# Performance work log

Measured on AMD Instinct MI355X. Metric: run time of the kernel, lower is better.

Reference implementation:

```python
import jax, jax.numpy as jnp
import numpy as np

VOCAB = 50257
K = 10  # accuracy_slack_size


def setup_inputs() -> dict:
    key = jax.random.key(0)
    k1, k2, k3, k4 = jax.random.split(key, 4)
    logits = jax.random.normal(k1, (4, 2048, 512), dtype=jnp.float32)
    target = jax.random.randint(k2, (4, 2048), 0, VOCAB, dtype=jnp.int64 if jax.config.jax_enable_x64 else jnp.int32)
    mask = jax.random.randint(k3, (4, 2048), 0, 2, dtype=jnp.int32)
    W = jax.random.normal(k4, (512, VOCAB), dtype=jnp.float32) * 0.02
    b = jnp.zeros((VOCAB,), dtype=jnp.float32)
    return {"logits": logits, "target": target, "mask": mask, "W": W, "b": b}


def reference(logits, target, mask, W, b):
    N = logits.shape[0] * logits.shape[1]
    x = logits.reshape(N, logits.shape[-1])            # [N, d]
    # sampled_softmax.log_prob: full log-softmax over vocab
    logp = jax.nn.log_softmax(x @ W + b, axis=-1)      # [N, V]
    _, words = jax.lax.top_k(logp, K)                  # [N, K] indices
    tgt = target.reshape(-1)                           # [N]
    msk = mask.reshape(-1).astype(jnp.float32)         # [N]
    # vectorized membership: is target among top-K predictions?
    hit = jnp.any(words == tgt[:, None], axis=1).astype(jnp.float32)
    counter = jnp.sum(hit * msk)
    all_counter = jnp.sum(msk)
    return jnp.array([counter / all_counter])
```

## Files before the change

### kernel.cpp

```cpp
#include <hip/hip_runtime.h>
#include <stdint.h>

#define V_VOCAB 50257
#define V_PAD   51200
#define NROWS   8192
#define DIM     512
#define KTOP    10
#define ACH     16

typedef __attribute__((ext_vector_type(8))) short  short8;
typedef __attribute__((ext_vector_type(4))) float  f32x4;
typedef __attribute__((ext_vector_type(4))) int    i32x4;
typedef __attribute__((ext_vector_type(2))) unsigned int u32x2;

struct Ctrl { int mc; int namb; int hits; int pad_; };

#define OFF_WT8    0ULL
#define SZ_WT8     26214400ULL
#define OFF_XQ8    (OFF_WT8 + SZ_WT8)
#define SZ_XQ8     4194304ULL
#define OFF_BPAD   (OFF_XQ8 + SZ_XQ8)
#define SZ_COL     (51200ULL*4)
#define OFF_SW8    (OFF_BPAD + SZ_COL)
#define OFF_W1     (OFF_SW8 + SZ_COL)
#define OFF_IVW    (OFF_W1 + SZ_COL)
#define OFF_ROWIDX (OFF_IVW + SZ_COL)
#define OFF_SXR    (OFF_ROWIDX + 32768ULL)
#define OFF_X1     (OFF_SXR + 32768ULL)
#define OFF_RMETA  (OFF_X1 + 32768ULL)
#define OFF_COUNTS (OFF_RMETA + 131072ULL)
#define OFF_AMB    (OFF_COUNTS + 32768ULL)
#define OFF_CTRL   (OFF_AMB + 32768ULL)
#define OFF_RK     (OFF_CTRL + 16ULL)
#define OFF_SST    (OFF_RK + 32768ULL)

#define GLOAD16(gp, lp) __builtin_amdgcn_global_load_lds( \
    (const __attribute__((address_space(1))) unsigned int*)(gp), \
    (__attribute__((address_space(3))) unsigned int*)(lp), 16, 0, 0)

__global__ void k_prep(const int* __restrict__ mask, const float* __restrict__ b,
                       float* __restrict__ bpad, int* __restrict__ rowidx,
                       Ctrl* __restrict__ ctrl) {
  int i = blockIdx.x * 256 + threadIdx.x;
  if (i < V_PAD) bpad[i] = (i < V_VOCAB) ? b[i] : -1e30f;
  if (i < NROWS && mask[i] != 0) {
    int p = atomicAdd(&ctrl->mc, 1);
    rowidx[p] = i;
  }
}

__global__ void k_wstat(const float* __restrict__ W, float* __restrict__ sw8,
                        float* __restrict__ w1, float* __restrict__ invw) {
  const int j = blockIdx.x * 256 + threadIdx.x;
  if (j >= V_PAD) return;
  if (j >= V_VOCAB) { sw8[j] = 1.f; w1[j] = 0.f; invw[j] = 0.f; return; }
  float am = 0.f, s1 = 0.f;
  for (int k = 0; k < DIM; ++k) {
    float v = fabsf(W[(size_t)k * V_VOCAB + j]);
    am = fmaxf(am, v);
    s1 += v;
  }
  sw8[j] = (am > 0.f) ? am / 126.f : 1.f;
  invw[j] = (am > 0.f) ? 126.f / am : 0.f;
  w1[j] = s1;
}

__global__ void k_twt8(const float* __restrict__ W, const float* __restrict__ invw,
                       signed char* __restrict__ Wt8) {
  __shared__ float lt[64][65];
  const int vbase = blockIdx.x * 64;
  const int kbase = blockIdx.y * 64;
  const int tid = threadIdx.x;
  const int krow = tid >> 6;
  const int col  = tid & 63;
  const int v    = vbase + col;
#pragma unroll
  for (int rr = 0; rr < 16; ++rr) {
    int kl = krow + rr * 4;
    float val = (v < V_VOCAB) ? W[(size_t)(kbase + kl) * V_VOCAB + v] : 0.0f;
    lt[kl][col] = val;
  }
  __syncthreads();
  const int vr = tid >> 3;
  const int kc = tid & 7;
#pragma unroll
  for (int p = 0; p < 2; ++p) {
    const int vl = p * 32 + vr;
    const float inv = invw[vbase + vl];
    unsigned int lo = 0, hi = 0;
#pragma unroll
    for (int j = 0; j < 4; ++j) {
      int q = (int)rintf(lt[kc * 8 + j][vl] * inv);
      lo |= ((unsigned int)(q & 255)) << (8 * j);
    }
#pragma unroll
    for (int j = 0; j < 4; ++j) {
      int q = (int)rintf(lt[kc * 8 + 4 + j][vl] * inv);
      hi |= ((unsigned int)(q & 255)) << (8 * j);
    }
    u32x2 t; t.x = lo; t.y = hi;
    *(u32x2*)(Wt8 + (size_t)(vbase + vl) * DIM + kbase + kc * 8) = t;
  }
}

__global__ void k_xq(const float* __restrict__ x, const int* __restrict__ rowidx,
                     const Ctrl* __restrict__ ctrl, signed char* __restrict__ Xq8,
                     float* __restrict__ sxr, float* __restrict__ x1) {
  const int wid = threadIdx.x >> 6, lane = threadIdx.x & 63;
  const int i = blockIdx.x * 4 + wid;
  const int mc = ctrl->mc;
  if (i >= mc) {
    u32x2 z; z.x = 0; z.y = 0;
    *(u32x2*)(Xq8 + (size_t)i * DIM + lane * 8) = z;
    if (lane == 0) { sxr[i] = 1.f; x1[i] = 0.f; }
    return;
  }
  const float* src = x + (size_t)rowidx[i] * DIM + lane * 8;
  float v[8];
  float am = 0.f, s1 = 0.f;
#pragma unroll
  for (int j = 0; j < 8; ++j) {
    v[j] = src[j];
    float a = fabsf(v[j]);
    am = fmaxf(am, a);
    s1 += a;
  }
#pragma unroll
  for (int d = 1; d < 64; d <<= 1) {
    am = fmaxf(am, __shfl_xor(am, d, 64));
    s1 += __shfl_xor(s1, d, 64);
  }
  const float sx  = (am > 0.f) ? am / 126.f : 1.f;
  const float inv = (am > 0.f) ? 126.f / am : 0.f;
  unsigned int lo = 0, hi = 0;
#pragma unroll
  for (int j = 0; j < 4; ++j) {
    int q = (int)rintf(v[j] * inv);
    lo |= ((unsigned int)(q & 255)) << (8 * j);
  }
#pragma unroll
  for (int j = 0; j < 4; ++j) {
    int q = (int)rintf(v[4 + j] * inv);
    hi |= ((unsigned int)(q & 255)) << (8 * j);
  }
  u32x2 t; t.x = lo; t.y = hi;
  *(u32x2*)(Xq8 + (size_t)i * DIM + lane * 8) = t;
  if (lane == 0) { sxr[i] = sx; x1[i] = s1; }
}

__global__ void k_that8(const signed char* __restrict__ Xq8,
                        const signed char* __restrict__ Wt8,
                        const float* __restrict__ bpad, const float* __restrict__ sw8,
                        const float* __restrict__ w1,
                        const float* __restrict__ sxr, const float* __restrict__ x1,
                        const int* __restrict__ rowidx, const int* __restrict__ target,
                        const Ctrl* __restrict__ ctrl, f32x4* __restrict__ rmeta) {
  const int wid = threadIdx.x >> 6, lane = threadIdx.x & 63;
  const int i = blockIdx.x * 4 + wid;
  const int mc = ctrl->mc;
  if (i >= mc) {
    if (lane == 0) { f32x4 rm; rm.x = 1.f; rm.y = 1e30f; rm.z = 0.f; rm.w = 0.f; rmeta[i] = rm; }
    return;
  }
  const int tg = target[rowidx[i]];
  u32x2 xq = *(const u32x2*)(Xq8 + (size_t)i * DIM + lane * 8);
  u32x2 wq = *(const u32x2*)(Wt8 + (size_t)tg * DIM + lane * 8);
  int d = 0;
#pragma unroll
  for (int j = 0; j < 4; ++j)
    d += (int)((signed char)(xq.x >> (8 * j))) * (int)((signed char)(wq.x >> (8 * j)));
#pragma unroll
  for (int j = 0; j < 4; ++j)
    d += (int)((signed char)(xq.y >> (8 * j))) * (int)((signed char)(wq.y >> (8 * j)));
#pragma unroll
  for (int dd = 1; dd < 64; dd <<= 1) d += __shfl_xor(d, dd, 64);
  if (lane == 0) {
    const float sx = sxr[i], sw = sw8[tg], xl1 = x1[i];
    f32x4 rm;
    rm.x = sx;
    rm.y = fmaf((float)d, sx * sw, bpad[tg]);
    rm.z = 0.5005f * (sx * w1[tg] + sw * xl1) + 128.5f * (sx * sw)
           + 1e-3f;
    rm.w = fmaf(128.5f, sx, 0.5005f * xl1);
    rmeta[i] = rm;
  }
}

__launch_bounds__(256, 4)
__global__ void k_count8(const signed char* __restrict__ Xq8,
                         const signed char* __restrict__ Wt8,
                         const float* __restrict__ bpad, const float* __restrict__ sw8,
                         const float* __restrict__ w1, const f32x4* __restrict__ rmeta,
                         const Ctrl* __restrict__ ctrl, unsigned int* __restrict__ counts) {
  const int mc = ctrl->mc;
  const int lin = blockIdx.x;
  const int xcd = lin & 7;
  const int idx = lin >> 3;
  const int mt  = xcd * 4 + (idx & 3);
  const int nt  = idx >> 2;
  const int nbase = nt * 64;

  __shared__ char lds[24576];

  const int tid  = threadIdx.x;
  const int lane = tid & 63;
  const int w    = tid >> 6;
  const int wr   = w >> 1;
  const int wc   = w & 1;

  const char* Bg = (const char*)Wt8 + (size_t)nbase * 512;
  const int r8   = tid >> 3;
  const int sws  = ((tid & 7) ^ (r8 & 7)) * 16;
  const int dst0 = tid * 16;

  const int fr = lane & 15;
  const int fq = lane >> 4;
  const int p0 = ((fq) ^ (fr & 7)) * 16;
  const int p1 = ((4 + fq) ^ (fr & 7)) * 16;

#define STAGE(Ag, kt) do {                                                     \
    const size_t _kb = (size_t)(kt) * 128;                                     \
    _Pragma("unroll") for (int _c = 0; _c < 4; ++_c)                           \
      GLOAD16((Ag) + (size_t)(_c * 32 + r8) * 512 + _kb + sws,                 \
              lds + _c * 4096 + dst0);                                         \
    _Pragma("unroll") for (int _c = 0; _c < 2; ++_c)                           \
      GLOAD16(Bg + (size_t)(_c * 32 + r8) * 512 + _kb + sws,                   \
              lds + 16384 + _c * 4096 + dst0);                                 \
  } while (0)

#define KTILE() do {                                                           \
    _Pragma("unroll") for (int _ks = 0; _ks < 2; ++_ks) {                      \
      const int _p = _ks ? p1 : p0;                                            \
      i32x4 a4[4], b2[2];                                                      \
      _Pragma("unroll") for (int _i = 0; _i < 4; ++_i)                         \
        a4[_i] = *(const i32x4*)(lds + (wr * 64 + _i * 16 + fr) * 128 + _p);   \
      _Pragma("unroll") for (int _i = 0; _i < 2; ++_i)                         \
        b2[_i] = *(const i32x4*)(lds + 16384 +                                 \
                                 (wc * 32 + _i * 16 + fr) * 128 + _p);         \
      __builtin_amdgcn_s_setprio(1);                                           \
      _Pragma("unroll") for (int _m = 0; _m < 4; ++_m)                         \
      _Pragma("unroll") for (int _n = 0; _n < 2; ++_n)                         \
        acc[_m][_n] = __builtin_amdgcn_mfma_i32_16x16x64_i8(                   \
            a4[_m], b2[_n], acc[_m][_n], 0, 0, 0);                             \
      __builtin_amdgcn_s_setprio(0);                                           \
    }                                                                          \
  } while (0)

  i32x4 acc[4][2];

  for (int mb = mt * 128; mb < mc; mb += 4096) {
    const char* Ag = (const char*)Xq8 + (size_t)mb * 512;
#pragma unroll
    for (int a = 0; a < 4; ++a)
#pragma unroll
      for (int c = 0; c < 2; ++c) acc[a][c] = (i32x4)0;

#pragma unroll
    for (int kt = 0; kt < 4; ++kt) {
      STAGE(Ag, kt);
      __syncthreads();
      KTILE();
      __syncthreads();
    }

    float bv[2], swc[2], w1c[2];
#pragma unroll
    for (int ni = 0; ni < 2; ++ni) {
      const int c = nbase + wc * 32 + ni * 16 + fr;
      bv[ni] = bpad[c]; swc[ni] = sw8[c]; w1c[ni] = w1[c];
    }

#pragma unroll
    for (int mi = 0; mi < 4; ++mi) {
#pragma unroll
      for (int r = 0; r < 4; ++r) {
        const int m = mb + wr * 64 + mi * 16 + fq * 4 + r;
        const f32x4 rm = rmeta[m];
        const float arr = 0.5005f * rm.x;
        unsigned int p = 0;
#pragma unroll
        for (int ni = 0; ni < 2; ++ni) {
          const float s  = fmaf((float)acc[mi][ni][r], rm.x * swc[ni], bv[ni]);
          const float mm = fmaf(arr, w1c[ni], fmaf(rm.w, swc[ni], rm.z));
          p += (s > rm.y - mm) ? 1u : 0u;
          p += (s > rm.y + mm) ? (1u << 16) : 0u;
        }
        int pi = (int)p;
#pragma unroll
        for (int d = 1; d < 16; d <<= 1) pi += __shfl_xor(pi, d, 64);
        if ((lane & 15) == 0) atomicAdd(&counts[m], (unsigned int)pi);
      }
    }
  }
#undef STAGE
#undef KTILE
}

__global__ void k_decide(const unsigned int* __restrict__ counts,
                         Ctrl* __restrict__ ctrl, int* __restrict__ amb) {
  const int i = blockIdx.x * 256 + threadIdx.x;
  if (i >= ctrl->mc) return;
  const unsigned int c = counts[i];
  const unsigned int lo = c & 0xFFFFu, hi = c >> 16;
  if (lo <= KTOP - 1) { atomicAdd(&ctrl->hits, 1); }
  else if (hi >= KTOP) {  }
  else { int p = atomicAdd(&ctrl->namb, 1); amb[p] = i; }
}

__global__ void k_fixt(const float* __restrict__ x, const float* __restrict__ W,
                       const float* __restrict__ b, const int* __restrict__ rowidx,
                       const int* __restrict__ target, const int* __restrict__ amb,
                       const Ctrl* __restrict__ ctrl, float* __restrict__ sst) {
  const int a = blockIdx.x * 64 + threadIdx.x;
  if (a >= ctrl->namb) return;
  const int n = rowidx[amb[a]];
  const int tg = target[n];
  float st = 0.f;
  for (int k = 0; k < DIM; ++k)
    st = fmaf(x[(size_t)n * DIM + k], W[(size_t)k * V_VOCAB + tg], st);
  sst[a] = st + b[tg];
}

__global__ void k_fixscan(const float* __restrict__ x, const float* __restrict__ W,
                          const float* __restrict__ b, const int* __restrict__ rowidx,
                          const int* __restrict__ target, const int* __restrict__ amb,
                          const float* __restrict__ sst, const Ctrl* __restrict__ ctrl,
                          int* __restrict__ rk) {
  __shared__ float sx[ACH][DIM];
  const int j = blockIdx.x * 256 + threadIdx.x;
  const int namb = ctrl->namb;
  const float bj = (j < V_VOCAB) ? b[j] : 0.f;
  for (int base = 0; base < namb; base += ACH) {
    __syncthreads();
    for (int t = threadIdx.x; t < ACH * DIM / 4; t += 256) {
      const int a  = t / (DIM / 4);
      const int kk = (t % (DIM / 4)) * 4;
      f32x4 v = (f32x4)0.f;
      if (base + a < namb) {
        const int n = rowidx[amb[base + a]];
        v = *(const f32x4*)(x + (size_t)n * DIM + kk);
      }
      *(f32x4*)(&sx[a][kk]) = v;
    }
    __syncthreads();
    if (j >= V_VOCAB) continue;
    float s[ACH];
#pragma unroll
    for (int a = 0; a < ACH; ++a) s[a] = 0.f;
    for (int k = 0; k < DIM; ++k) {
      const float wv = W[(size_t)k * V_VOCAB + j];
#pragma unroll
      for (int a = 0; a < ACH; ++a) s[a] = fmaf(sx[a][k], wv, s[a]);
    }
#pragma unroll
    for (int a = 0; a < ACH; ++a) {
      if (base + a < namb) {
        const int tg = target[rowidx[amb[base + a]]];
        const float sc = s[a] + bj;
        const float st = sst[base + a];
        if (sc > st || (sc == st && j < tg)) atomicAdd(&rk[base + a], 1);
      }
    }
  }
}

__global__ void k_fixdec(const int* __restrict__ rk, Ctrl* __restrict__ ctrl) {
  const int a = blockIdx.x * 256 + threadIdx.x;
  if (a < ctrl->namb && rk[a] <= KTOP - 1) atomicAdd(&ctrl->hits, 1);
}

__global__ void k_final(const Ctrl* __restrict__ ctrl, float* __restrict__ out) {
  out[0] = (float)ctrl->hits / (float)ctrl->mc;
}

extern "C" void kernel_launch(void* const* d_in, const int* in_sizes, int n_in,
                              void* d_out, int out_size, void* d_ws, size_t ws_size,
                              hipStream_t stream) {
  const float* x      = (const float*)d_in[0];
  const int*   target = (const int*)d_in[1];
  const int*   mask   = (const int*)d_in[2];
  const float* W      = (const float*)d_in[3];
  const float* b      = (const float*)d_in[4];
  float* out = (float*)d_out;

  char* ws = (char*)d_ws;
  signed char*    Wt8    = (signed char*)(ws + OFF_WT8);
  signed char*    Xq8    = (signed char*)(ws + OFF_XQ8);
  float*          bpad   = (float*)(ws + OFF_BPAD);
  float*          sw8    = (float*)(ws + OFF_SW8);
  float*          w1     = (float*)(ws + OFF_W1);
  float*          invw   = (float*)(ws + OFF_IVW);
  int*            rowidx = (int*)(ws + OFF_ROWIDX);
  float*          sxr    = (float*)(ws + OFF_SXR);
  float*          x1     = (float*)(ws + OFF_X1);
  f32x4*          rmeta  = (f32x4*)(ws + OFF_RMETA);
  unsigned int*   counts = (unsigned int*)(ws + OFF_COUNTS);
  int*            amb    = (int*)(ws + OFF_AMB);
  Ctrl*           ctrl   = (Ctrl*)(ws + OFF_CTRL);
  int*            rk     = (int*)(ws + OFF_RK);
  float*          sst    = (float*)(ws + OFF_SST);

  hipMemsetAsync(ws + OFF_COUNTS, 0, 32768 + 32768 + 16 + 32768, stream);

  k_prep   <<<200, 256, 0, stream>>>(mask, b, bpad, rowidx, ctrl);
  k_wstat  <<<200, 256, 0, stream>>>(W, sw8, w1, invw);
  k_twt8   <<<dim3(800, 8), 256, 0, stream>>>(W, invw, Wt8);
  k_xq     <<<2048, 256, 0, stream>>>(x, rowidx, ctrl, Xq8, sxr, x1);
  k_that8  <<<2048, 256, 0, stream>>>(Xq8, Wt8, bpad, sw8, w1, sxr, x1,
                                      rowidx, target, ctrl, rmeta);
  k_count8 <<<25600, 256, 0, stream>>>(Xq8, Wt8, bpad, sw8, w1, rmeta,
                                       ctrl, counts);
  k_decide <<<32, 256, 0, stream>>>(counts, ctrl, amb);
  k_fixt   <<<128, 64, 0, stream>>>(x, W, b, rowidx, target, amb, ctrl, sst);
  k_fixscan<<<197, 256, 0, stream>>>(x, W, b, rowidx, target, amb, sst, ctrl, rk);
  k_fixdec <<<32, 256, 0, stream>>>(rk, ctrl);
  k_final  <<<1, 1, 0, stream>>>(ctrl, out);
}
```

Baseline: 507.6 us.

## Keep W tiles register-resident in MFMA fragment layout and stream X rows

The quantized W matrix is now written directly in MFMA B-fragment order, so each count-kernel block loads its 128-column W slice into registers once and keeps it there. The block then streams 128-row X tiles through a larger swizzled LDS buffer and runs the full K=512 product without per-k-tile synchronisation. The grid shrinks from 25600 to 1600 persistent-style blocks, each looping over a quarter of the rows, and the per-column bias and scale loads are hoisted out of the row loop. This cuts repeated W loads and barriers, at the cost of many more registers and LDS per block, lowering occupancy to 2 blocks per CU. The target-gather kernel is updated to read from the new fragment layout.

New measurement: 853.4 us. +68.1%, slower.

```diff
diff --git a/kernel.cpp b/kernel.cpp
--- a/kernel.cpp
+++ b/kernel.cpp
@@ -65,8 +65,8 @@
   w1[j] = s1;
 }
 
-__global__ void k_twt8(const float* __restrict__ W, const float* __restrict__ invw,
-                       signed char* __restrict__ Wt8) {
+__global__ void k_twt8f(const float* __restrict__ W, const float* __restrict__ invw,
+                        signed char* __restrict__ Wt8f) {
   __shared__ float lt[64][65];
   const int vbase = blockIdx.x * 64;
   const int kbase = blockIdx.y * 64;
@@ -77,30 +77,27 @@
 #pragma unroll
   for (int rr = 0; rr < 16; ++rr) {
     int kl = krow + rr * 4;
-    float val = (v < V_VOCAB) ? W[(size_t)(kbase + kl) * V_VOCAB + v] : 0.0f;
-    lt[kl][col] = val;
+    lt[kl][col] = (v < V_VOCAB) ? W[(size_t)(kbase + kl) * V_VOCAB + v] : 0.0f;
   }
   __syncthreads();
-  const int vr = tid >> 3;
-  const int kc = tid & 7;
-#pragma unroll
-  for (int p = 0; p < 2; ++p) {
-    const int vl = p * 32 + vr;
-    const float inv = invw[vbase + vl];
-    unsigned int lo = 0, hi = 0;
+  const int cb_l = tid >> 6;
+  const int lane = tid & 63;
+  const int col_l = cb_l * 16 + (lane & 15);
+  const float inv = invw[vbase + col_l];
+  const int k0 = (lane >> 4) * 16;
+  unsigned int out[4];
+#pragma unroll
+  for (int q = 0; q < 4; ++q) {
+    unsigned int a = 0;
 #pragma unroll
     for (int j = 0; j < 4; ++j) {
-      int q = (int)rintf(lt[kc * 8 + j][vl] * inv);
-      lo |= ((unsigned int)(q & 255)) << (8 * j);
-    }
-#pragma unroll
-    for (int j = 0; j < 4; ++j) {
-      int q = (int)rintf(lt[kc * 8 + 4 + j][vl] * inv);
-      hi |= ((unsigned int)(q & 255)) << (8 * j);
-    }
-    u32x2 t; t.x = lo; t.y = hi;
-    *(u32x2*)(Wt8 + (size_t)(vbase + vl) * DIM + kbase + kc * 8) = t;
-  }
+      int qq = (int)rintf(lt[k0 + q * 4 + j][col_l] * inv);
+      a |= ((unsigned int)(qq & 255)) << (8 * j);
+    }
+    out[q] = a;
+  }
+  const size_t chunk = (size_t)((vbase >> 4) + cb_l) * 8 + blockIdx.y;
+  *(i32x4*)(Wt8f + (chunk * 64 + lane) * 16) = *(i32x4*)out;
 }
 
 __global__ void k_xq(const float* __restrict__ x, const int* __restrict__ rowidx,
@@ -149,7 +146,7 @@
 }
 
 __global__ void k_that8(const signed char* __restrict__ Xq8,
-                        const signed char* __restrict__ Wt8,
+                        const signed char* __restrict__ Wt8f,
                         const float* __restrict__ bpad, const float* __restrict__ sw8,
                         const float* __restrict__ w1,
                         const float* __restrict__ sxr, const float* __restrict__ x1,
@@ -163,8 +160,11 @@
     return;
   }
   const int tg = target[rowidx[i]];
+  const int cchunk = (tg >> 4) * 8 + (lane >> 3);
+  const int l_in   = ((lane >> 1) & 3) * 16 + (tg & 15);
+  const int jo     = (lane & 1) * 8;
   u32x2 xq = *(const u32x2*)(Xq8 + (size_t)i * DIM + lane * 8);
-  u32x2 wq = *(const u32x2*)(Wt8 + (size_t)tg * DIM + lane * 8);
+  u32x2 wq = *(const u32x2*)(Wt8f + ((size_t)cchunk * 64 + l_in) * 16 + jo);
   int d = 0;
 #pragma unroll
   for (int j = 0; j < 4; ++j)
@@ -186,9 +186,9 @@
   }
 }
 
-__launch_bounds__(256, 4)
-__global__ void k_count8(const signed char* __restrict__ Xq8,
-                         const signed char* __restrict__ Wt8,
+__launch_bounds__(256, 2)
+__global__ void k_countB(const signed char* __restrict__ Xq8,
+                         const signed char* __restrict__ Wt8f,
                          const float* __restrict__ bpad, const float* __restrict__ sw8,
                          const float* __restrict__ w1, const f32x4* __restrict__ rmeta,
                          const Ctrl* __restrict__ ctrl, unsigned int* __restrict__ counts) {
@@ -196,85 +196,72 @@
   const int lin = blockIdx.x;
   const int xcd = lin & 7;
   const int idx = lin >> 3;
-  const int mt  = xcd * 4 + (idx & 3);
-  const int nt  = idx >> 2;
-  const int nbase = nt * 64;
-
-  __shared__ char lds[24576];
+  const int mg  = idx & 3;
+  const int nt  = xcd * 50 + (idx >> 2);
+  const int nbase = nt * 128;
+
+  __shared__ char lds[65536];
 
   const int tid  = threadIdx.x;
   const int lane = tid & 63;
   const int w    = tid >> 6;
-  const int wr   = w >> 1;
-  const int wc   = w & 1;
-
-  const char* Bg = (const char*)Wt8 + (size_t)nbase * 512;
-  const int r8   = tid >> 3;
-  const int sws  = ((tid & 7) ^ (r8 & 7)) * 16;
-  const int dst0 = tid * 16;
-
   const int fr = lane & 15;
   const int fq = lane >> 4;
-  const int p0 = ((fq) ^ (fr & 7)) * 16;
-  const int p1 = ((4 + fq) ^ (fr & 7)) * 16;
-
-#define STAGE(Ag, kt) do {                                                     \
-    const size_t _kb = (size_t)(kt) * 128;                                     \
-    _Pragma("unroll") for (int _c = 0; _c < 4; ++_c)                           \
-      GLOAD16((Ag) + (size_t)(_c * 32 + r8) * 512 + _kb + sws,                 \
-              lds + _c * 4096 + dst0);                                         \
-    _Pragma("unroll") for (int _c = 0; _c < 2; ++_c)                           \
-      GLOAD16(Bg + (size_t)(_c * 32 + r8) * 512 + _kb + sws,                   \
-              lds + 16384 + _c * 4096 + dst0);                                 \
-  } while (0)
-
-#define KTILE() do {                                                           \
-    _Pragma("unroll") for (int _ks = 0; _ks < 2; ++_ks) {                      \
-      const int _p = _ks ? p1 : p0;                                            \
-      i32x4 a4[4], b2[2];                                                      \
-      _Pragma("unroll") for (int _i = 0; _i < 4; ++_i)                         \
-        a4[_i] = *(const i32x4*)(lds + (wr * 64 + _i * 16 + fr) * 128 + _p);   \
-      _Pragma("unroll") for (int _i = 0; _i < 2; ++_i)                         \
-        b2[_i] = *(const i32x4*)(lds + 16384 +                                 \
-                                 (wc * 32 + _i * 16 + fr) * 128 + _p);         \
-      __builtin_amdgcn_s_setprio(1);                                           \
-      _Pragma("unroll") for (int _m = 0; _m < 4; ++_m)                         \
-      _Pragma("unroll") for (int _n = 0; _n < 2; ++_n)                         \
-        acc[_m][_n] = __builtin_amdgcn_mfma_i32_16x16x64_i8(                   \
-            a4[_m], b2[_n], acc[_m][_n], 0, 0, 0);                             \
-      __builtin_amdgcn_s_setprio(0);                                           \
-    }                                                                          \
-  } while (0)
-
-  i32x4 acc[4][2];
-
-  for (int mb = mt * 128; mb < mc; mb += 4096) {
+
+  const int cb0 = nt * 8 + w * 2;
+  i32x4 breg[2][8];
+#pragma unroll
+  for (int ni = 0; ni < 2; ++ni)
+#pragma unroll
+    for (int ks = 0; ks < 8; ++ks)
+      breg[ni][ks] = *(const i32x4*)(Wt8f +
+          ((size_t)((cb0 + ni) * 8 + ks) * 64 + lane) * 16);
+
+  float bv[2], swc[2], w1c[2];
+#pragma unroll
+  for (int ni = 0; ni < 2; ++ni) {
+    const int c = nbase + w * 32 + ni * 16 + fr;
+    bv[ni] = bpad[c]; swc[ni] = sw8[c]; w1c[ni] = w1[c];
+  }
+
+  i32x4 acc[8][2];
+
+  for (int mb = mg * 128; mb < mc; mb += 512) {
     const char* Ag = (const char*)Xq8 + (size_t)mb * 512;
 #pragma unroll
-    for (int a = 0; a < 4; ++a)
-#pragma unroll
-      for (int c = 0; c < 2; ++c) acc[a][c] = (i32x4)0;
-
-#pragma unroll
-    for (int kt = 0; kt < 4; ++kt) {
-      STAGE(Ag, kt);
-      __syncthreads();
-      KTILE();
-      __syncthreads();
-    }
-
-    float bv[2], swc[2], w1c[2];
-#pragma unroll
-    for (int ni = 0; ni < 2; ++ni) {
-      const int c = nbase + wc * 32 + ni * 16 + fr;
-      bv[ni] = bpad[c]; swc[ni] = sw8[c]; w1c[ni] = w1[c];
-    }
-
-#pragma unroll
-    for (int mi = 0; mi < 4; ++mi) {
+    for (int u = 0; u < 16; ++u) {
+      const int D = u * 256 + tid;
+      const int row = D >> 5, slot = D & 31;
+      GLOAD16(Ag + (size_t)row * 512 + (size_t)((slot ^ (row & 15)) * 16),
+              lds + D * 16);
+    }
+    __syncthreads();
+
+#pragma unroll
+    for (int a = 0; a < 8; ++a) { acc[a][0] = (i32x4)0; acc[a][1] = (i32x4)0; }
+
+    __builtin_amdgcn_s_setprio(1);
+#pragma unroll
+    for (int ks = 0; ks < 8; ++ks) {
+#pragma unroll
+      for (int mi = 0; mi < 8; ++mi) {
+        const int row  = mi * 16 + fr;
+        const int phys = (ks * 4 + fq) ^ fr;
+        i32x4 a4 = *(const i32x4*)(lds + row * 512 + phys * 16);
+        acc[mi][0] = __builtin_amdgcn_mfma_i32_16x16x64_i8(
+            a4, breg[0][ks], acc[mi][0], 0, 0, 0);
+        acc[mi][1] = __builtin_amdgcn_mfma_i32_16x16x64_i8(
+            a4, breg[1][ks], acc[mi][1], 0, 0, 0);
+      }
+    }
+    __builtin_amdgcn_s_setprio(0);
+    __syncthreads();
+
+#pragma unroll
+    for (int mi = 0; mi < 8; ++mi) {
 #pragma unroll
       for (int r = 0; r < 4; ++r) {
-        const int m = mb + wr * 64 + mi * 16 + fq * 4 + r;
+        const int m = mb + mi * 16 + fq * 4 + r;
         const f32x4 rm = rmeta[m];
         const float arr = 0.5005f * rm.x;
         unsigned int p = 0;
@@ -292,8 +279,6 @@
       }
     }
   }
-#undef STAGE
-#undef KTILE
 }
 
 __global__ void k_decide(const unsigned int* __restrict__ counts,
@@ -384,7 +369,7 @@
   float* out = (float*)d_out;
 
   char* ws = (char*)d_ws;
-  signed char*    Wt8    = (signed char*)(ws + OFF_WT8);
+  signed char*    Wt8f   = (signed char*)(ws + OFF_WT8);
   signed char*    Xq8    = (signed char*)(ws + OFF_XQ8);
   float*          bpad   = (float*)(ws + OFF_BPAD);
   float*          sw8    = (float*)(ws + OFF_SW8);
@@ -404,12 +389,12 @@
 
   k_prep   <<<200, 256, 0, stream>>>(mask, b, bpad, rowidx, ctrl);
   k_wstat  <<<200, 256, 0, stream>>>(W, sw8, w1, invw);
-  k_twt8   <<<dim3(800, 8), 256, 0, stream>>>(W, invw, Wt8);
+  k_twt8f  <<<dim3(800, 8), 256, 0, stream>>>(W, invw, Wt8f);
   k_xq     <<<2048, 256, 0, stream>>>(x, rowidx, ctrl, Xq8, sxr, x1);
-  k_that8  <<<2048, 256, 0, stream>>>(Xq8, Wt8, bpad, sw8, w1, sxr, x1,
+  k_that8  <<<2048, 256, 0, stream>>>(Xq8, Wt8f, bpad, sw8, w1, sxr, x1,
                                       rowidx, target, ctrl, rmeta);
-  k_count8 <<<25600, 256, 0, stream>>>(Xq8, Wt8, bpad, sw8, w1, rmeta,
-                                       ctrl, counts);
+  k_countB <<<1600, 256, 0, stream>>>(Xq8, Wt8f, bpad, sw8, w1, rmeta,
+                                      ctrl, counts);
   k_decide <<<32, 256, 0, stream>>>(counts, ctrl, amb);
   k_fixt   <<<128, 64, 0, stream>>>(x, W, b, rowidx, target, amb, ctrl, sst);
   k_fixscan<<<197, 256, 0, stream>>>(x, W, b, rowidx, target, amb, sst, ctrl, rk);
```
